# Kernel optimization log

Hardware: AMD Instinct MI355X
Metric: run time of the kernel (lower is better)

Reference implementation:

```python
import jax, jax.numpy as jnp
import numpy as np

B, S, D, H = 128, 512, 512, 4
DH = D // H

def setup_inputs() -> dict:
    key = jax.random.key(0)
    ks = jax.random.split(key, 12)
    s = 1.0 / np.sqrt(D)
    inp = {
        "x": jax.random.normal(ks[0], (B, S, D), dtype=jnp.float32),
        "Wi": jax.random.uniform(ks[1], (D, D), jnp.float32, -s, s),
        "bi": jnp.zeros((D,), jnp.float32),
        "Wq": jax.random.uniform(ks[2], (D, D), jnp.float32, -s, s),
        "bq": jnp.zeros((D,), jnp.float32),
        "Wk": jax.random.uniform(ks[3], (D, D), jnp.float32, -s, s),
        "bk": jnp.zeros((D,), jnp.float32),
        "Wv": jax.random.uniform(ks[4], (D, D), jnp.float32, -s, s),
        "bv": jnp.zeros((D,), jnp.float32),
        "Wo": jax.random.uniform(ks[5], (D, D), jnp.float32, -s, s),
        "bo": jnp.zeros((D,), jnp.float32),
        "data_lens": jax.random.randint(ks[6], (B,), 1, S + 1, dtype=jnp.int32),
    }
    return inp


def _forward(x, Wi, bi, Wq, bq, Wk, bk, Wv, bv, Wo, bo, data_lens):
    # fc_i applied to the whole sequence up front
    xf = x @ Wi + bi                      # [B, S, D]
    h0 = xf[:, 0, :]                      # initial state = fc_i(x)[:, 0]
    scale = 1.0 / jnp.sqrt(jnp.asarray(DH, xf.dtype))

    def step(h, x_t):
        # h: [B, D] previous state (acts as key and value, kv_len == 1)
        # x_t: [B, D] current input (query)
        q = (x_t @ Wq + bq).reshape(B, H, DH)
        k = (h @ Wk + bk).reshape(B, H, DH)
        v = (h @ Wv + bv).reshape(B, H, DH)
        scores = jnp.sum(q * k, axis=-1, keepdims=True) * scale   # [B, H, 1]
        w = jax.nn.softmax(scores, axis=-1)                       # == 1 (single key)
        attn = (w * v).reshape(B, D)
        h_new = attn @ Wo + bo + x_t                              # residual
        return h_new, h_new

    xs = jnp.transpose(xf, (1, 0, 2))     # [S, B, D]
    _, outs = jax.lax.scan(step, h0, xs)  # [S, B, D]
    outputs = jnp.transpose(outs, (1, 0, 2))                      # [B, S, D]

    idx = (data_lens.astype(jnp.int32) - 1)[:, None, None]        # [B,1,1]
    final_state = jnp.take_along_axis(outputs, idx, axis=1)[:, 0, :]
    return outputs, final_state


def reference(x, Wi, bi, Wq, bq, Wk, bk, Wv, bv, Wo, bo, data_lens):
    return _forward(x, Wi, bi, Wq, bq, Wk, bk, Wv, bv, Wo, bo, data_lens)
```

## Files before the change

kernel.cpp:

```cpp
#include <hip/hip_runtime.h>
#include <hip/hip_bf16.h>

typedef __hip_bfloat16 bf16;
typedef __attribute__((ext_vector_type(8))) short short8;
typedef __attribute__((ext_vector_type(4))) float f32x4;

#define S_LEN 512
#define DIM   512
#define BATCH 128
#define ROWS  (BATCH * S_LEN)

__device__ inline unsigned short f2bu(float f){
    bf16 h = __float2bfloat16(f);
    return *reinterpret_cast<unsigned short*>(&h);
}
__device__ inline float ld_in(const void* p, size_t i, int f32){
    return f32 ? ((const float*)p)[i] : __bfloat162float(((const bf16*)p)[i]);
}

typedef __attribute__((address_space(1))) const unsigned int gu32;
typedef __attribute__((address_space(3))) unsigned int lu32;
__device__ __forceinline__ void gld16(const void* g, void* l){
    __builtin_amdgcn_global_load_lds((gu32*)g, (lu32*)l, 16, 0, 0);
}

__device__ __forceinline__ short8 lds_frag(const unsigned short* base, int row, int koff){
    const unsigned off = ((unsigned)(row*128 + koff*2)) ^ (((unsigned)(row & 7)) << 4);
    return *(const short8*)((const char*)base + off);
}

__global__ void detect_dtype(const unsigned int* __restrict__ x, int* __restrict__ flag)
{
    __shared__ int cnt;
    if (threadIdx.x == 0) cnt = 0;
    __syncthreads();
    int loc = 0;
    for (int i = threadIdx.x; i < 8192; i += 256)
        if (((x[i] >> 7) & 0xFFu) == 0xFFu) loc++;
    atomicAdd(&cnt, loc);
    __syncthreads();
    if (threadIdx.x == 0) *flag = (cnt > 0) ? 1 : 0;
}

__global__ void conv_tr(const void* __restrict__ in, bf16* __restrict__ outp,
                        const int* __restrict__ flagp)
{
    const int f32 = *flagp;
    __shared__ unsigned short tile[32][33];
    const int bx = blockIdx.x, by = blockIdx.y;
    const int tx = threadIdx.x, ty = threadIdx.y;
    #pragma unroll
    for (int j = 0; j < 32; j += 8)
        tile[ty + j][tx] = f2bu(ld_in(in, (size_t)(by*32 + ty + j)*DIM + bx*32 + tx, f32));
    __syncthreads();
    #pragma unroll
    for (int j = 0; j < 32; j += 8) {
        unsigned short u = tile[tx][ty + j];
        outp[(size_t)(bx*32 + ty + j)*DIM + by*32 + tx] = *reinterpret_cast<bf16*>(&u);
    }
}

__global__ void conv_cp(const void* __restrict__ in, bf16* __restrict__ outp,
                        const int* __restrict__ flagp)
{
    const int f32 = *flagp;
    const size_t i = (size_t)blockIdx.x*256 + threadIdx.x;
    outp[i] = __float2bfloat16(ld_in(in, i, f32));
}

__global__ void conv_x(const void* __restrict__ X, size_t eoff, bf16* __restrict__ xb,
                       const int* __restrict__ flagp)
{
    const int f32 = *flagp;
    const size_t i = ((size_t)blockIdx.x*256 + threadIdx.x)*8;
    if (f32) {
        const float* p = (const float*)X + eoff + i;
        float4 a = *(const float4*)p;
        float4 b = *(const float4*)(p + 4);
        __align__(16) unsigned short wv[8];
        wv[0]=f2bu(a.x); wv[1]=f2bu(a.y); wv[2]=f2bu(a.z); wv[3]=f2bu(a.w);
        wv[4]=f2bu(b.x); wv[5]=f2bu(b.y); wv[6]=f2bu(b.z); wv[7]=f2bu(b.w);
        *(uint4*)(xb + i) = *(const uint4*)wv;
    } else {
        *(uint4*)(xb + i) = *(const uint4*)((const bf16*)X + eoff + i);
    }
}

__global__ void cvec_kernel(const bf16* __restrict__ WoT, const void* __restrict__ bv,
                            const void* __restrict__ bo, const void* __restrict__ bi,
                            const int* __restrict__ flagp,
                            float* __restrict__ dvec, float* __restrict__ bvec)
{
    const int f32 = *flagp;
    const int n = blockIdx.x * 4 + (threadIdx.x >> 6);
    const int lane = threadIdx.x & 63;
    float acc = 0.f;
    for (int k = lane; k < DIM; k += 64)
        acc += ld_in(bv, k, f32) * __bfloat162float(WoT[(size_t)n*DIM + k]);
    #pragma unroll
    for (int o = 32; o > 0; o >>= 1) acc += __shfl_down(acc, o, 64);
    if (lane == 0) {
        const float dd = acc + ld_in(bo, n, f32);
        dvec[n] = dd;
        bvec[n] = dd + ld_in(bi, n, f32);
    }
}

__global__ void prep_aux(const float* __restrict__ U0, const float* __restrict__ V0,
                         const float* __restrict__ dvec,
                         bf16* __restrict__ A1, bf16* __restrict__ V0b, bf16* __restrict__ Zr)
{
    const int idx = blockIdx.x * 256 + threadIdx.x;
    const int n = idx & 511;
    A1[idx]  = __float2bfloat16(U0[idx] - dvec[n]);
    V0b[idx] = __float2bfloat16(V0[idx]);
    if (idx < 512) Zr[idx] = __float2bfloat16(0.f);
}

#define TILE_PROLOGUE                                                          \
    __shared__ __align__(16) unsigned short As[128][72];                       \
    __shared__ __align__(16) unsigned short Bs[128][72];                       \
    const int tid  = threadIdx.x;                                              \
    const int lane = tid & 63;                                                 \
    const int wave = tid >> 6;                                                 \
    const int wm = (wave & 1) * 64;                                            \
    const int wn = (wave >> 1) * 64;                                           \
    const int cn = lane & 15;                                                  \
    const int quad = lane >> 4;                                                \
    f32x4 acc[4][4];                                                           \
    _Pragma("unroll")                                                          \
    for (int i = 0; i < 4; ++i)                                                \
        _Pragma("unroll")                                                      \
        for (int j = 0; j < 4; ++j) acc[i][j] = (f32x4){0.f,0.f,0.f,0.f};

#define TILE_MFMA                                                              \
        __syncthreads();                                                       \
        _Pragma("unroll")                                                      \
        for (int ks = 0; ks < 64; ks += 32) {                                  \
            short8 af[4], bfr[4];                                              \
            const int koff = ks + quad*8;                                      \
            _Pragma("unroll")                                                  \
            for (int i = 0; i < 4; ++i) af[i]  = *(const short8*)&As[wm + i*16 + cn][koff]; \
            _Pragma("unroll")                                                  \
            for (int j = 0; j < 4; ++j) bfr[j] = *(const short8*)&Bs[wn + j*16 + cn][koff]; \
            _Pragma("unroll")                                                  \
            for (int i = 0; i < 4; ++i)                                        \
                _Pragma("unroll")                                              \
                for (int j = 0; j < 4; ++j)                                    \
                    acc[i][j] = __builtin_amdgcn_mfma_f32_16x16x32_bf16(af[i], bfr[j], acc[i][j], 0, 0, 0); \
        }                                                                      \
        __syncthreads();

#define STAGE_B(Bt, C0)                                                        \
        {                                                                      \
            int r = tid >> 3; const int c = (tid & 7) * 8;                     \
            _Pragma("unroll")                                                  \
            for (int p = 0; p < 4; ++p, r += 32) {                             \
                uint4 v = *(const uint4*)((Bt) + (size_t)((C0) + r)*DIM + k0 + c); \
                *(uint4*)&Bs[r][c] = v;                                        \
            }                                                                  \
        }

#define STAGE_A_IN(SRC, BASE)                                                  \
                if (f32) {                                                     \
                    const float* sp = (const float*)(SRC) + (BASE);            \
                    float4 a = *(const float4*)sp;                             \
                    float4 b = *(const float4*)(sp + 4);                       \
                    __align__(16) unsigned short w[8];                         \
                    w[0]=f2bu(a.x); w[1]=f2bu(a.y); w[2]=f2bu(a.z); w[3]=f2bu(a.w); \
                    w[4]=f2bu(b.x); w[5]=f2bu(b.y); w[6]=f2bu(b.z); w[7]=f2bu(b.w); \
                    *(uint4*)&As[r][c] = *(const uint4*)w;                     \
                } else {                                                       \
                    *(uint4*)&As[r][c] = *(const uint4*)((const bf16*)(SRC) + (BASE)); \
                }

__global__ __launch_bounds__(256) void gemm_sq(const bf16* __restrict__ A,
        const bf16* __restrict__ Btm, bf16* __restrict__ Pout, bf16* __restrict__ Tout)
{
    TILE_PROLOGUE
    const int R0 = blockIdx.y * 128;
    const int C0 = blockIdx.x * 128;
    for (int k0 = 0; k0 < DIM; k0 += 64) {
        {
            int r = tid >> 3; const int c = (tid & 7) * 8;
            #pragma unroll
            for (int p = 0; p < 4; ++p, r += 32)
                *(uint4*)&As[r][c] = *(const uint4*)(A + (size_t)(R0 + r)*DIM + k0 + c);
        }
        STAGE_B(Btm, C0)
        TILE_MFMA
    }
    #pragma unroll
    for (int i = 0; i < 4; ++i) {
        const int rowb = R0 + wm + i*16 + quad*4;
        #pragma unroll
        for (int j = 0; j < 4; ++j) {
            const int cc = C0 + wn + j*16 + cn;
            #pragma unroll
            for (int rr = 0; rr < 4; ++rr) {
                const float v = acc[i][j][rr];
                Pout[(size_t)(rowb + rr)*DIM + cc] = __float2bfloat16(v);
                Tout[(size_t)cc*DIM + rowb + rr]  = __float2bfloat16(v);
            }
        }
    }
}

__global__ __launch_bounds__(256) void gemm_row0(const void* __restrict__ X,
        const bf16* __restrict__ WiT, const float* __restrict__ bvec,
        const int* __restrict__ flagp, float* __restrict__ U0)
{
    const int f32 = *flagp;
    TILE_PROLOGUE
    const int C0 = blockIdx.x * 128;
    for (int k0 = 0; k0 < DIM; k0 += 64) {
        {
            int r = tid >> 3; const int c = (tid & 7) * 8;
            #pragma unroll
            for (int p = 0; p < 4; ++p, r += 32) {
                const size_t base = (size_t)r*S_LEN*DIM + k0 + c;
                STAGE_A_IN(X, base)
            }
        }
        STAGE_B(WiT, C0)
        TILE_MFMA
    }
    #pragma unroll
    for (int i = 0; i < 4; ++i) {
        const int rowb = wm + i*16 + quad*4;
        #pragma unroll
        for (int j = 0; j < 4; ++j) {
            const int cc = C0 + wn + j*16 + cn;
            const float bb = bvec[cc];
            #pragma unroll
            for (int rr = 0; rr < 4; ++rr)
                U0[(size_t)(rowb + rr)*DIM + cc] = acc[i][j][rr] + bb;
        }
    }
}

__global__ __launch_bounds__(256) void gemm_v0(const float* __restrict__ U0,
        const bf16* __restrict__ T0, const float* __restrict__ dvec, float* __restrict__ V0)
{
    TILE_PROLOGUE
    const int C0 = blockIdx.x * 128;
    for (int k0 = 0; k0 < DIM; k0 += 64) {
        {
            int r = tid >> 3; const int c = (tid & 7) * 8;
            #pragma unroll
            for (int p = 0; p < 4; ++p, r += 32) {
                __align__(16) unsigned short w[8];
                #pragma unroll
                for (int q = 0; q < 8; ++q)
                    w[q] = f2bu(U0[(size_t)r*DIM + k0 + c + q] - dvec[k0 + c + q]);
                *(uint4*)&As[r][c] = *(const uint4*)w;
            }
        }
        STAGE_B(T0, C0)
        TILE_MFMA
    }
    #pragma unroll
    for (int i = 0; i < 4; ++i) {
        const int rowb = wm + i*16 + quad*4;
        #pragma unroll
        for (int j = 0; j < 4; ++j) {
            const int cc = C0 + wn + j*16 + cn;
            #pragma unroll
            for (int rr = 0; rr < 4; ++rr) {
                const size_t off = (size_t)(rowb + rr)*DIM + cc;
                V0[off] = acc[i][j][rr] + U0[off];
            }
        }
    }
}

template<int MODE, bool TO_OUT>
__global__ __launch_bounds__(256, 2) void gemm_big(
        const bf16* __restrict__ Abf, const bf16* __restrict__ A1,
        const bf16* __restrict__ V0b, const bf16* __restrict__ Zr,
        const bf16* __restrict__ Bt,  const float* __restrict__ Rf,
        float* __restrict__ Of, bf16* __restrict__ Ob,
        void* __restrict__ Oout, size_t eoff, const int* __restrict__ flagp,
        const int shift)
{
    __shared__ __align__(16) unsigned short As[3][64*64];
    __shared__ __align__(16) unsigned short Bs[3][128*64];
    const int tid  = threadIdx.x;
    const int lane = tid & 63;
    const int w    = tid >> 6;
    const int nb = gridDim.x;
    const int p0 = blockIdx.x;
    const int L  = (p0 & 7) * (nb >> 3) + (p0 >> 3);
    const int bx = L & 3, by = L >> 2;
    const int R0 = by * 64, C0 = bx * 128;
    const int wm = (w & 1) * 32;
    const int wn = (w >> 1) * 64;
    const int cn = lane & 15;
    const int quad = lane >> 4;
    f32x4 acc[2][4];
    #pragma unroll
    for (int i = 0; i < 2; ++i)
        #pragma unroll
        for (int j = 0; j < 4; ++j) acc[i][j] = (f32x4){0.f,0.f,0.f,0.f};

    const int lr  = w*8 + (lane >> 3);
    const int lcb = ((lane & 7) ^ (lane >> 3)) * 8;
    const int ldst = w * 512;
    const bf16* aln[2];
    const bf16* bln[4];
    #pragma unroll
    for (int l = 0; l < 2; ++l) {
        const int grow = R0 + l*32 + lr;
        const bf16* a;
        if (MODE == 2) {
            a = Abf + (size_t)grow*DIM;
        } else if (MODE == 1) {
            const int t = grow & (S_LEN - 1);
            if      (t == 0) a = A1  + (size_t)(grow >> 9)*DIM;
            else if (t == 1) a = V0b + (size_t)(grow >> 9)*DIM;
            else             a = Abf + (size_t)(grow - 1)*DIM;
        } else {
            const int t = grow & (S_LEN - 1);
            a = (t >= shift) ? (Abf + (size_t)(grow - shift)*DIM) : Zr;
        }
        aln[l] = a + lcb;
    }
    #pragma unroll
    for (int l = 0; l < 4; ++l)
        bln[l] = Bt + (size_t)(C0 + l*32 + lr)*DIM + lcb;

#define STAGE(SLOT, KN)                                                        \
    {                                                                          \
        gld16(aln[0] + (KN), &As[SLOT][0*2048 + ldst]);                        \
        gld16(aln[1] + (KN), &As[SLOT][1*2048 + ldst]);                        \
        gld16(bln[0] + (KN), &Bs[SLOT][0*2048 + ldst]);                        \
        gld16(bln[1] + (KN), &Bs[SLOT][1*2048 + ldst]);                        \
        gld16(bln[2] + (KN), &Bs[SLOT][2*2048 + ldst]);                        \
        gld16(bln[3] + (KN), &Bs[SLOT][3*2048 + ldst]);                        \
    }

    STAGE(0, 0)
    STAGE(1, 64)
    STAGE(2, 128)

#define STEP(U, VM)                                                            \
    {                                                                          \
        asm volatile("s_waitcnt vmcnt(" #VM ")" ::: "memory");                 \
        __builtin_amdgcn_s_barrier();                                          \
        const unsigned short* Ac = &As[(U) % 3][0];                            \
        const unsigned short* Bc = &Bs[(U) % 3][0];                            \
        short8 af[2][2], bfr[4][2];                                            \
        _Pragma("unroll")                                                      \
        for (int i = 0; i < 2; ++i) {                                          \
            af[i][0] = lds_frag(Ac, wm + i*16 + cn,      quad*8);              \
            af[i][1] = lds_frag(Ac, wm + i*16 + cn, 32 + quad*8);              \
        }                                                                      \
        _Pragma("unroll")                                                      \
        for (int j = 0; j < 4; ++j) {                                          \
            bfr[j][0] = lds_frag(Bc, wn + j*16 + cn,      quad*8);             \
            bfr[j][1] = lds_frag(Bc, wn + j*16 + cn, 32 + quad*8);             \
        }                                                                      \
        _Pragma("unroll")                                                      \
        for (int i = 0; i < 2; ++i)                                            \
            _Pragma("unroll")                                                  \
            for (int j = 0; j < 4; ++j) {                                      \
                acc[i][j] = __builtin_amdgcn_mfma_f32_16x16x32_bf16(af[i][0], bfr[j][0], acc[i][j], 0, 0, 0); \
                acc[i][j] = __builtin_amdgcn_mfma_f32_16x16x32_bf16(af[i][1], bfr[j][1], acc[i][j], 0, 0, 0); \
            }                                                                  \
        __builtin_amdgcn_s_barrier();                                          \
        if ((U) + 3 < 8) STAGE((U) % 3, ((U) + 3) * 64)                        \
    }

    STEP(0, 12)
    STEP(1, 12)
    STEP(2, 12)
    STEP(3, 12)
    STEP(4, 12)
    STEP(5, 12)
    STEP(6, 6)
    STEP(7, 0)
#undef STEP
#undef STAGE

    const int f32o = TO_OUT ? *flagp : 0;
    #pragma unroll
    for (int i = 0; i < 2; ++i) {
        const int rowb = R0 + wm + i*16 + quad*4;
        #pragma unroll
        for (int j = 0; j < 4; ++j) {
            const int cc = C0 + wn + j*16 + cn;
            #pragma unroll
            for (int rr = 0; rr < 4; ++rr) {
                const size_t off = (size_t)(rowb + rr)*DIM + cc;
                const float res = (MODE == 2) ? Rf[cc] : Rf[off];
                const float v = acc[i][j][rr] + res;
                if (TO_OUT) {
                    if (f32o) ((float*)Oout)[eoff + off] = v;
                    else      ((bf16*)Oout)[eoff + off]  = __float2bfloat16(v);
                } else {
                    Of[off] = v;
                    Ob[off] = __float2bfloat16(v);
                }
            }
        }
    }
}

__global__ void gather_final(void* __restrict__ out, const int* __restrict__ lens,
                             const int* __restrict__ flagp)
{
    const int f32 = *flagp;
    const int idx = blockIdx.x * 256 + threadIdx.x;
    const int b = idx >> 9, n = idx & 511;
    int L = lens[b];
    if (L < 1) L = 1;
    if (L > S_LEN) L = S_LEN;
    const size_t src = ((size_t)b*S_LEN + (L - 1))*DIM + n;
    const size_t dst = (size_t)ROWS*DIM + idx;
    if (f32) ((float*)out)[dst] = ((const float*)out)[src];
    else     ((bf16*)out)[dst]  = ((const bf16*)out)[src];
}

extern "C" void kernel_launch(void* const* d_in, const int* in_sizes, int n_in,
                              void* d_out, int out_size, void* d_ws, size_t ws_size,
                              hipStream_t stream)
{
    const void* X  = d_in[0];
    const void* Wi = d_in[1];
    const void* bi = d_in[2];
    const void* Wv = d_in[7];
    const void* bv = d_in[8];
    const void* Wo = d_in[9];
    const void* bo = d_in[10];
    const int* lens = (const int*)d_in[11];
    char* ws = (char*)d_ws;

    const size_t MATB = (size_t)DIM * DIM * sizeof(bf16);
    bf16* WiT = (bf16*)(ws + 0*MATB);
    bf16* WoT = (bf16*)(ws + 1*MATB);
    bf16* Wvb = (bf16*)(ws + 2*MATB);
    bf16* S2  = (bf16*)(ws + 3*MATB);
    bf16* S3  = (bf16*)(ws + 4*MATB);
    bf16* T0  = (bf16*)(ws + 5*MATB);
    bf16* T1  = (bf16*)(ws + 6*MATB);
    bf16* T2  = (bf16*)(ws + 7*MATB);
    bf16* T3  = (bf16*)(ws + 8*MATB);
    size_t off = 9*MATB;
    float* dvec = (float*)(ws + off); off += 2048;
    float* bvec = (float*)(ws + off); off += 2048;
    int*   flag = (int*)  (ws + off); off += 256;
    float* U0   = (float*)(ws + off); off += (size_t)BATCH*DIM*4;
    float* V0   = (float*)(ws + off); off += (size_t)BATCH*DIM*4;
    bf16*  A1   = (bf16*) (ws + off); off += (size_t)BATCH*DIM*2;
    bf16*  V0b  = (bf16*) (ws + off); off += (size_t)BATCH*DIM*2;
    bf16*  Zr   = (bf16*) (ws + off); off += 1024;
    off = (off + 1023) & ~(size_t)1023;
    char* dyn = ws + off;
    const size_t avail = ws_size > off ? ws_size - off : 0;

    int CR = 512;
    for (long cr = 65536; cr >= 512; cr >>= 1)
        if ((size_t)cr * 7168 <= avail) { CR = (int)cr; break; }

    bf16*  xbf = (bf16*) dyn;
    float* Uf  = (float*)(dyn + (size_t)CR*1024);
    bf16*  Ub  = (bf16*) (dyn + (size_t)CR*3072);
    float* Vf  = (float*)(dyn + (size_t)CR*4096);
    bf16*  Vb  = (bf16*) (dyn + (size_t)CR*6144);

    detect_dtype<<<1, 256, 0, stream>>>((const unsigned int*)X, flag);
    conv_tr<<<dim3(16,16), dim3(32,8), 0, stream>>>(Wi, WiT, flag);
    conv_tr<<<dim3(16,16), dim3(32,8), 0, stream>>>(Wo, WoT, flag);
    conv_cp<<<1024, 256, 0, stream>>>(Wv, Wvb, flag);
    cvec_kernel<<<128, 256, 0, stream>>>(WoT, bv, bo, bi, flag, dvec, bvec);
    gemm_sq<<<dim3(4,4), 256, 0, stream>>>(Wvb, WoT, S2, T0);
    gemm_sq<<<dim3(4,4), 256, 0, stream>>>(S2, T0, S3, T1);
    gemm_sq<<<dim3(4,4), 256, 0, stream>>>(S3, T1, S2, T2);
    gemm_sq<<<dim3(4,4), 256, 0, stream>>>(S2, T2, S3, T3);
    gemm_row0<<<dim3(4,1), 256, 0, stream>>>(X, WiT, bvec, flag, U0);
    gemm_v0<<<dim3(4,1), 256, 0, stream>>>(U0, T0, dvec, V0);
    prep_aux<<<256, 256, 0, stream>>>(U0, V0, dvec, A1, V0b, Zr);

    const int NC = ROWS / CR;
    const int nb = (CR / 64) * 4;
    for (int c = 0; c < NC; ++c) {
        const size_t eoff = (size_t)c*CR*DIM;
        const size_t boff = (size_t)(c*(CR/S_LEN))*DIM;
        conv_x<<<CR/4, 256, 0, stream>>>(X, eoff, xbf, flag);
        gemm_big<2,false><<<nb, 256, 0, stream>>>(xbf, nullptr, nullptr, Zr,
                WiT, bvec, Uf, Ub, nullptr, 0, flag, 0);
        gemm_big<1,false><<<nb, 256, 0, stream>>>(Ub, A1 + boff, V0b + boff, Zr,
                T0, Uf, Vf, Vb, nullptr, 0, flag, 1);
        gemm_big<0,false><<<nb, 256, 0, stream>>>(Vb, nullptr, nullptr, Zr,
                T1, Vf, Uf, Ub, nullptr, 0, flag, 2);
        gemm_big<0,false><<<nb, 256, 0, stream>>>(Ub, nullptr, nullptr, Zr,
                T2, Uf, Vf, Vb, nullptr, 0, flag, 4);
        gemm_big<0,true ><<<nb, 256, 0, stream>>>(Vb, nullptr, nullptr, Zr,
                T3, Vf, nullptr, nullptr, d_out, eoff, flag, 8);
    }
    gather_final<<<256, 256, 0, stream>>>(d_out, lens, flag);
}
```

Baseline: 1.023 ms.

## Replace triple-buffered LDS DMA with register-prefetched single-buffer pipeline in gemm_big

The big GEMM kernel stops using three LDS stages filled by global_load_lds and instead prefetches two K-tiles into registers, writing each into a single LDS buffer just before it is computed. This cuts shared memory per block roughly threefold, which allows raising launch bounds to 4 blocks per CU for more occupancy. It also switches to an XOR-swizzled LDS layout and sets wave priority around the MFMA section. In exchange, the kernel uses more VGPRs for the staging registers and serializes the LDS write with compute through extra barriers and an lgkmcnt wait, which may expose latency.

```diff
diff --git a/kernel.cpp b/kernel.cpp
--- a/kernel.cpp
+++ b/kernel.cpp
@@ -275,7 +275,7 @@
 }
 
 template<int MODE, bool TO_OUT>
-__global__ __launch_bounds__(256, 2) void gemm_big(
+__global__ __launch_bounds__(256, 4) void gemm_big(
         const bf16* __restrict__ Abf, const bf16* __restrict__ A1,
         const bf16* __restrict__ V0b, const bf16* __restrict__ Zr,
         const bf16* __restrict__ Bt,  const float* __restrict__ Rf,
@@ -283,8 +283,8 @@
         void* __restrict__ Oout, size_t eoff, const int* __restrict__ flagp,
         const int shift)
 {
-    __shared__ __align__(16) unsigned short As[3][64*64];
-    __shared__ __align__(16) unsigned short Bs[3][128*64];
+    __shared__ __align__(16) unsigned short As[64*64];
+    __shared__ __align__(16) unsigned short Bs[128*64];
     const int tid  = threadIdx.x;
     const int lane = tid & 63;
     const int w    = tid >> 6;
@@ -303,84 +303,108 @@
         #pragma unroll
         for (int j = 0; j < 4; ++j) acc[i][j] = (f32x4){0.f,0.f,0.f,0.f};
 
-    const int lr  = w*8 + (lane >> 3);
-    const int lcb = ((lane & 7) ^ (lane >> 3)) * 8;
-    const int ldst = w * 512;
-    const bf16* aln[2];
-    const bf16* bln[4];
-    #pragma unroll
-    for (int l = 0; l < 2; ++l) {
-        const int grow = R0 + l*32 + lr;
-        const bf16* a;
-        if (MODE == 2) {
-            a = Abf + (size_t)grow*DIM;
-        } else if (MODE == 1) {
-            const int t = grow & (S_LEN - 1);
-            if      (t == 0) a = A1  + (size_t)(grow >> 9)*DIM;
-            else if (t == 1) a = V0b + (size_t)(grow >> 9)*DIM;
-            else             a = Abf + (size_t)(grow - 1)*DIM;
-        } else {
-            const int t = grow & (S_LEN - 1);
-            a = (t >= shift) ? (Abf + (size_t)(grow - shift)*DIM) : Zr;
-        }
-        aln[l] = a + lcb;
-    }
-    #pragma unroll
-    for (int l = 0; l < 4; ++l)
-        bln[l] = Bt + (size_t)(C0 + l*32 + lr)*DIM + lcb;
-
-#define STAGE(SLOT, KN)                                                        \
-    {                                                                          \
-        gld16(aln[0] + (KN), &As[SLOT][0*2048 + ldst]);                        \
-        gld16(aln[1] + (KN), &As[SLOT][1*2048 + ldst]);                        \
-        gld16(bln[0] + (KN), &Bs[SLOT][0*2048 + ldst]);                        \
-        gld16(bln[1] + (KN), &Bs[SLOT][1*2048 + ldst]);                        \
-        gld16(bln[2] + (KN), &Bs[SLOT][2*2048 + ldst]);                        \
-        gld16(bln[3] + (KN), &Bs[SLOT][3*2048 + ldst]);                        \
-    }
-
-    STAGE(0, 0)
-    STAGE(1, 64)
-    STAGE(2, 128)
-
-#define STEP(U, VM)                                                            \
+    const int lr = w*8 + (lane >> 3);
+    const int ce = (lane & 7) * 8;
+    const bf16* aln0; const bf16* aln1;
+    const bf16* bln0; const bf16* bln1; const bf16* bln2; const bf16* bln3;
+    {
+        const bf16* ap[2];
+        #pragma unroll
+        for (int l = 0; l < 2; ++l) {
+            const int grow = R0 + l*32 + lr;
+            const bf16* a;
+            if (MODE == 2) {
+                a = Abf + (size_t)grow*DIM;
+            } else if (MODE == 1) {
+                const int t = grow & (S_LEN - 1);
+                if      (t == 0) a = A1  + (size_t)(grow >> 9)*DIM;
+                else if (t == 1) a = V0b + (size_t)(grow >> 9)*DIM;
+                else             a = Abf + (size_t)(grow - 1)*DIM;
+            } else {
+                const int t = grow & (S_LEN - 1);
+                a = (t >= shift) ? (Abf + (size_t)(grow - shift)*DIM) : Zr;
+            }
+            ap[l] = a + ce;
+        }
+        aln0 = ap[0]; aln1 = ap[1];
+        bln0 = Bt + (size_t)(C0 +  0 + lr)*DIM + ce;
+        bln1 = Bt + (size_t)(C0 + 32 + lr)*DIM + ce;
+        bln2 = Bt + (size_t)(C0 + 64 + lr)*DIM + ce;
+        bln3 = Bt + (size_t)(C0 + 96 + lr)*DIM + ce;
+    }
+    const unsigned swz = ((unsigned)(lr & 7)) << 4;
+    const unsigned cby = ((unsigned)ce * 2) ^ swz;
+    const unsigned adst0 = (unsigned)(( 0 + lr)*128) + cby;
+    const unsigned adst1 = (unsigned)((32 + lr)*128) + cby;
+    const unsigned bdst0 = (unsigned)(( 0 + lr)*128) + cby;
+    const unsigned bdst1 = (unsigned)((32 + lr)*128) + cby;
+    const unsigned bdst2 = (unsigned)((64 + lr)*128) + cby;
+    const unsigned bdst3 = (unsigned)((96 + lr)*128) + cby;
+
+    uint4 ea0, ea1, eb0, eb1, eb2, eb3;
+    uint4 oa0, oa1, ob0, ob1, ob2, ob3;
+
+#define ISSUE(P, KN)                                                           \
+    P##a0 = *(const uint4*)(aln0 + (KN));                                      \
+    P##a1 = *(const uint4*)(aln1 + (KN));                                      \
+    P##b0 = *(const uint4*)(bln0 + (KN));                                      \
+    P##b1 = *(const uint4*)(bln1 + (KN));                                      \
+    P##b2 = *(const uint4*)(bln2 + (KN));                                      \
+    P##b3 = *(const uint4*)(bln3 + (KN));
+
+#define LWRITE(P)                                                              \
+    *(uint4*)((char*)As + adst0) = P##a0;                                      \
+    *(uint4*)((char*)As + adst1) = P##a1;                                      \
+    *(uint4*)((char*)Bs + bdst0) = P##b0;                                      \
+    *(uint4*)((char*)Bs + bdst1) = P##b1;                                      \
+    *(uint4*)((char*)Bs + bdst2) = P##b2;                                      \
+    *(uint4*)((char*)Bs + bdst3) = P##b3;
+
+#define COMPUTE                                                                \
+    __builtin_amdgcn_s_setprio(1);                                             \
+    _Pragma("unroll")                                                          \
+    for (int ks = 0; ks < 64; ks += 32) {                                      \
+        short8 af[2], bfr[4];                                                  \
+        const int koff = ks + quad*8;                                          \
+        _Pragma("unroll")                                                      \
+        for (int i = 0; i < 2; ++i) af[i]  = lds_frag(As, wm + i*16 + cn, koff); \
+        _Pragma("unroll")                                                      \
+        for (int j = 0; j < 4; ++j) bfr[j] = lds_frag(Bs, wn + j*16 + cn, koff); \
+        _Pragma("unroll")                                                      \
+        for (int i = 0; i < 2; ++i)                                            \
+            _Pragma("unroll")                                                  \
+            for (int j = 0; j < 4; ++j)                                        \
+                acc[i][j] = __builtin_amdgcn_mfma_f32_16x16x32_bf16(af[i], bfr[j], acc[i][j], 0, 0, 0); \
+    }                                                                          \
+    __builtin_amdgcn_s_setprio(0);
+
+#define STEP(U, P, VM)                                                         \
     {                                                                          \
         asm volatile("s_waitcnt vmcnt(" #VM ")" ::: "memory");                 \
         __builtin_amdgcn_s_barrier();                                          \
-        const unsigned short* Ac = &As[(U) % 3][0];                            \
-        const unsigned short* Bc = &Bs[(U) % 3][0];                            \
-        short8 af[2][2], bfr[4][2];                                            \
-        _Pragma("unroll")                                                      \
-        for (int i = 0; i < 2; ++i) {                                          \
-            af[i][0] = lds_frag(Ac, wm + i*16 + cn,      quad*8);              \
-            af[i][1] = lds_frag(Ac, wm + i*16 + cn, 32 + quad*8);              \
-        }                                                                      \
-        _Pragma("unroll")                                                      \
-        for (int j = 0; j < 4; ++j) {                                          \
-            bfr[j][0] = lds_frag(Bc, wn + j*16 + cn,      quad*8);             \
-            bfr[j][1] = lds_frag(Bc, wn + j*16 + cn, 32 + quad*8);             \
-        }                                                                      \
-        _Pragma("unroll")                                                      \
-        for (int i = 0; i < 2; ++i)                                            \
-            _Pragma("unroll")                                                  \
-            for (int j = 0; j < 4; ++j) {                                      \
-                acc[i][j] = __builtin_amdgcn_mfma_f32_16x16x32_bf16(af[i][0], bfr[j][0], acc[i][j], 0, 0, 0); \
-                acc[i][j] = __builtin_amdgcn_mfma_f32_16x16x32_bf16(af[i][1], bfr[j][1], acc[i][j], 0, 0, 0); \
-            }                                                                  \
+        LWRITE(P)                                                              \
+        if ((U) + 2 < 8) { ISSUE(P, ((U) + 2) * 64) }                          \
+        asm volatile("s_waitcnt lgkmcnt(0)" ::: "memory");                     \
+        __builtin_amdgcn_sched_barrier(0);                                     \
         __builtin_amdgcn_s_barrier();                                          \
-        if ((U) + 3 < 8) STAGE((U) % 3, ((U) + 3) * 64)                        \
-    }
-
-    STEP(0, 12)
-    STEP(1, 12)
-    STEP(2, 12)
-    STEP(3, 12)
-    STEP(4, 12)
-    STEP(5, 12)
-    STEP(6, 6)
-    STEP(7, 0)
+        COMPUTE                                                                \
+    }
+
+    ISSUE(e, 0)
+    ISSUE(o, 64)
+
+    STEP(0, e, 6)
+    STEP(1, o, 6)
+    STEP(2, e, 6)
+    STEP(3, o, 6)
+    STEP(4, e, 6)
+    STEP(5, o, 6)
+    STEP(6, e, 6)
+    STEP(7, o, 0)
 #undef STEP
-#undef STAGE
+#undef COMPUTE
+#undef LWRITE
+#undef ISSUE
 
     const int f32o = TO_OUT ? *flagp : 0;
     #pragma unroll
```

Result: slower. 1.104 ms (+8.0%).
